# Optimization experiments

Hardware: AMD Instinct MI355X
Metric: run time of the kernel (lower is better)

## Reference

```python
import jax, jax.numpy as jnp
import numpy as np

B, N, C = 32, 262144, 5
ALPHA = 50.0
EPS_LS = 0.2
BASE_W = [0.8, 2.0, 1.5, 1.5, 3.5]
# (cid, ref, sign): height_diff = sign*(pr_z[cid] - gt_z[ref]); violation = sigmoid(-10*diff)
# Enumerates all z_above / z_below pairs in the hierarchy dict.
PAIRS = [(1, 2, -1.0), (1, 3, -1.0), (1, 4, -1.0),
         (2, 1, 1.0), (2, 3, -1.0), (2, 4, -1.0),
         (3, 1, 1.0), (3, 2, 1.0), (3, 4, -1.0),
         (4, 1, 1.0), (4, 2, 1.0), (4, 3, 1.0)]


def setup_inputs() -> dict:
    key = jax.random.key(0)
    k1, k2, k3 = jax.random.split(key, 3)
    outputs = jax.random.normal(k1, (B, C, N), dtype=jnp.float32)
    labels = jax.random.randint(k2, (B, N), 0, C, dtype=jnp.int32)
    points = jax.random.normal(k3, (B, N, 3), dtype=jnp.float32)
    return {"outputs": outputs, "labels": labels, "points": points}


def _centroid(points, mask):
    # points: [B,N,3], mask: [B,N] bool -> ([B,3], [B] valid)
    valid = mask.any(axis=1)
    m = mask.astype(points.dtype)
    s = jnp.einsum('bn,bnd->bd', m, points)
    cnt = jnp.clip(m.sum(axis=1), 1.0)
    return s / cnt[:, None], valid


def _forward(outputs, points, labels):
    logits = jnp.transpose(outputs, (0, 2, 1))  # [B,N,C]
    b = labels.shape[0]
    preds = jnp.argmax(logits, axis=-1)  # [B,N]
    base = jnp.asarray(BASE_W, dtype=logits.dtype)
    weights = jnp.broadcast_to(base, (b, C))
    gt_c = {cid: _centroid(points, labels == cid) for cid in (1, 2, 3, 4)}
    pr_c = {cid: _centroid(points, preds == cid) for cid in (1, 2, 3, 4)}
    # hierarchy violation scatter into per-batch class weights
    for cid, ref, sign in PAIRS:
        pr_pos, pos_valid = pr_c[cid]
        gt_ref, ref_valid = gt_c[ref]
        valid = ref_valid & pos_valid
        diff = sign * (pr_pos[:, 2] - gt_ref[:, 2])
        add = jnp.where(valid, ALPHA * jax.nn.sigmoid(-diff * 10.0), 0.0)
        weights = weights.at[:, cid].add(add).at[:, ref].add(0.3 * add)
    # predicted bounding boxes of masked points (zeros included, as in torch)
    bounds = {}
    for cid in (2, 3):
        mp = points * (preds == cid)[:, :, None].astype(points.dtype)
        bounds[cid] = jnp.stack([mp.min(axis=1), mp.max(axis=1)], axis=1)  # [B,2,3]
    for cid in (2, 3):
        rb = bounds[3 if cid == 2 else 2]
        xc = (bounds[cid][:, :, 0] - rb[:, 0:1, 0]) / (rb[:, 1:2, 0] - rb[:, 0:1, 0] + 1e-7)
        yc = (bounds[cid][:, :, 1] - rb[:, 0:1, 1]) / (rb[:, 1:2, 1] - rb[:, 0:1, 1] + 1e-7)
        viol = ((xc < 0.1) | (xc > 0.9)) | ((yc < 0.1) | (yc > 0.9))
        weights = weights.at[:, cid].add(ALPHA * viol.astype(weights.dtype).mean(axis=1))
    weights = jnp.clip(weights, 0.1, 10.0)
    # inverse-sqrt class frequency weights
    dist = jnp.bincount(labels.reshape(-1), length=C).astype(logits.dtype)
    cw = 1.0 / (jnp.sqrt(dist) + 1e-7)
    cw = cw / cw.sum() * C
    w = weights.mean(axis=0) * cw  # [C]
    # weighted cross entropy with label_smoothing=0.2 (PyTorch semantics)
    logp = jax.nn.log_softmax(logits.reshape(-1, C), axis=-1)
    y = labels.reshape(-1)
    wt = w[y]
    wsum = wt.sum()
    nll = (wt * -jnp.take_along_axis(logp, y[:, None], axis=1)[:, 0]).sum() / wsum
    smooth = (-(logp * w[None, :]).sum(axis=-1)).sum() / wsum
    return (1.0 - EPS_LS) * nll + (EPS_LS / C) * smooth


def reference(outputs, labels, points):
    return _forward(outputs, points, labels)
```

## Files before the change

### kernel.cpp

```cpp
#include <hip/hip_runtime.h>
#include <math.h>

#define NPTS 262144
#define BATCH 32
#define BPB 64
#define NBLK (BATCH * BPB)
#define NREP 8


__device__ __forceinline__ float wred_sum(float v) {
#pragma unroll
    for (int o = 32; o; o >>= 1) v += __shfl_down(v, o);
    return v;
}
__device__ __forceinline__ unsigned wred_usum(unsigned v) {
#pragma unroll
    for (int o = 32; o; o >>= 1) v += __shfl_down(v, o);
    return v;
}

__device__ __forceinline__ unsigned mapf(float f) {
    unsigned u = __float_as_uint(f);
    return (u & 0x80000000u) ? ~u : (u | 0x80000000u);
}
__device__ __forceinline__ float unmapf(unsigned m) {
    return (m & 0x80000000u) ? __uint_as_float(m ^ 0x80000000u)
                             : __uint_as_float(~m);
}

__global__ __launch_bounds__(256) void bsl_main(
    const float* __restrict__ outputs, const int* __restrict__ labels,
    const float* __restrict__ points,
    float* gsum, unsigned* gcnt, float* bsum, unsigned* bcnt,
    unsigned* bmn, unsigned* bmx, int iters)
{
    const int blk = blockIdx.x;
    const int b = blk / BPB;
    const int seg = blk % BPB;
    const int seg_start = seg * (iters * 1024);
    const int tid = threadIdx.x;

    float S[5] = {0, 0, 0, 0, 0};
    float T[5] = {0, 0, 0, 0, 0};
    float lseacc = 0.f;
    float gtz[4] = {0, 0, 0, 0};
    float prz[4] = {0, 0, 0, 0};
    const float INF = __int_as_float(0x7f800000);
    float mn2x = INF, mx2x = -INF, mn2y = INF, mx2y = -INF;
    float mn3x = INF, mx3x = -INF, mn3y = INF, mx3y = -INF;
    unsigned bc[5] = {0, 0, 0, 0, 0}, prc[4] = {0, 0, 0, 0};

    const float* obase = outputs + (size_t)b * 5 * NPTS;
    const int*   lbase = labels + (size_t)b * NPTS;
    const float* pbase = points + (size_t)b * NPTS * 3;

    for (int it = 0; it < iters; ++it) {
        const int n = seg_start + it * 1024 + tid * 4;
        float4 L[5];
#pragma unroll
        for (int c = 0; c < 5; ++c)
            L[c] = *(const float4*)(obase + (size_t)c * NPTS + n);
        const int4 lab = *(const int4*)(lbase + n);
        const float4* pp = (const float4*)(pbase + (size_t)n * 3);
        const float4 p0 = pp[0], p1 = pp[1], p2 = pp[2];
        const float xs[4] = {p0.x, p0.w, p1.z, p2.y};
        const float ys[4] = {p0.y, p1.x, p1.w, p2.z};
        const float zs[4] = {p0.z, p1.y, p2.x, p2.w};
        const int   lb[4] = {lab.x, lab.y, lab.z, lab.w};
#pragma unroll
        for (int j = 0; j < 4; ++j) {
            float v[5];
#pragma unroll
            for (int c = 0; c < 5; ++c) v[c] = ((const float*)&L[c])[j];
            float best = v[0]; int pred = 0;
#pragma unroll
            for (int c = 1; c < 5; ++c)
                if (v[c] > best) { best = v[c]; pred = c; }
            float e = 0.f;
#pragma unroll
            for (int c = 0; c < 5; ++c) e += __expf(v[c] - best);
            const float lse = best + __logf(e);
            lseacc += lse;
            const int y = lb[j];
#pragma unroll
            for (int c = 0; c < 5; ++c) {
                S[c] += v[c];
                const bool is = (y == c);
                T[c] += is ? (lse - v[c]) : 0.f;
                bc[c] += is ? 1u : 0u;
            }
            const float z = zs[j];
#pragma unroll
            for (int k = 0; k < 4; ++k) {
                const bool gy = (y == k + 1), py = (pred == k + 1);
                gtz[k] += gy ? z : 0.f;
                prz[k] += py ? z : 0.f;
                prc[k] += py ? 1u : 0u;
            }
            const float x = xs[j], yv = ys[j];
            const float a2x = (pred == 2) ? x : 0.f;
            const float a2y = (pred == 2) ? yv : 0.f;
            const float a3x = (pred == 3) ? x : 0.f;
            const float a3y = (pred == 3) ? yv : 0.f;
            mn2x = fminf(mn2x, a2x); mx2x = fmaxf(mx2x, a2x);
            mn2y = fminf(mn2y, a2y); mx2y = fmaxf(mx2y, a2y);
            mn3x = fminf(mn3x, a3x); mx3x = fmaxf(mx3x, a3x);
            mn3y = fminf(mn3y, a3y); mx3y = fmaxf(mx3y, a3y);
        }
    }

    float fv[27] = {S[0], S[1], S[2], S[3], S[4],
                    T[0], T[1], T[2], T[3], T[4],
                    lseacc,
                    gtz[0], gtz[1], gtz[2], gtz[3],
                    prz[0], prz[1], prz[2], prz[3],
                    mn2x, mx2x, mn2y, mx2y, mn3x, mx3x, mn3y, mx3y};
    unsigned iv[9] = {bc[0], bc[1], bc[2], bc[3], bc[4],
                      prc[0], prc[1], prc[2], prc[3]};

    __shared__ float sf[4][27];
    __shared__ unsigned si[4][9];
    const int wid = tid >> 6, lane = tid & 63;
#pragma unroll
    for (int vdx = 0; vdx < 27; ++vdx) {
        float r;
        if (vdx < 19) r = wred_sum(fv[vdx]);
        else if (((vdx - 19) & 1) == 0) {
#pragma unroll
            for (int o = 32; o; o >>= 1) fv[vdx] = fminf(fv[vdx], __shfl_down(fv[vdx], o));
            r = fv[vdx];
        } else {
#pragma unroll
            for (int o = 32; o; o >>= 1) fv[vdx] = fmaxf(fv[vdx], __shfl_down(fv[vdx], o));
            r = fv[vdx];
        }
        if (lane == 0) sf[wid][vdx] = r;
    }
#pragma unroll
    for (int vdx = 0; vdx < 9; ++vdx) {
        unsigned r = wred_usum(iv[vdx]);
        if (lane == 0) si[wid][vdx] = r;
    }
    __syncthreads();

    const int rep = blk & (NREP - 1);
    if (tid < 27) {
        float r = sf[0][tid];
        if (tid < 19) {
            r += sf[1][tid] + sf[2][tid] + sf[3][tid];
        } else if (((tid - 19) & 1) == 0) {
            r = fminf(fminf(r, sf[1][tid]), fminf(sf[2][tid], sf[3][tid]));
        } else {
            r = fmaxf(fmaxf(r, sf[1][tid]), fmaxf(sf[2][tid], sf[3][tid]));
        }
        if (tid < 11) {
            atomicAdd(&gsum[rep * 11 + tid], r);
        } else if (tid < 19) {
            atomicAdd(&bsum[b * 8 + (tid - 11)], r);
        } else {
            const int g = tid - 19;
            const unsigned m = mapf(r);
            if ((g & 1) == 0) atomicMin(&bmn[b * 4 + (g >> 1)], m);
            else              atomicMax(&bmx[b * 4 + (g >> 1)], m);
        }
    } else if (tid >= 32 && tid < 41) {
        const int v = tid - 32;
        const unsigned r = si[0][v] + si[1][v] + si[2][v] + si[3][v];
        if (v < 5) {
            atomicAdd(&gcnt[rep * 5 + v], r);
            if (v >= 1) atomicAdd(&bcnt[b * 8 + (v - 1)], r);
        } else {
            atomicAdd(&bcnt[b * 8 + 4 + (v - 5)], r);
        }
    }
}

__global__ __launch_bounds__(64) void bsl_final(
    const float* __restrict__ gsum, const unsigned* __restrict__ gcnt,
    const float* __restrict__ bsum, const unsigned* __restrict__ bcnt,
    const unsigned* __restrict__ bmn, const unsigned* __restrict__ bmx,
    float* __restrict__ out)
{
    const int lane = threadIdx.x;
    __shared__ float smg[16];

    if (lane < 16) {
        float s = 0.f;
        if (lane < 11) {
#pragma unroll
            for (int r = 0; r < NREP; ++r) s += gsum[r * 11 + lane];
        } else {
            unsigned u = 0;
#pragma unroll
            for (int r = 0; r < NREP; ++r) u += gcnt[r * 5 + (lane - 11)];
            s = (float)u;
        }
        smg[lane] = s;
    }

    const float BASE_W[5] = {0.8f, 2.0f, 1.5f, 1.5f, 3.5f};
    const int pc[12]  = {1, 1, 1, 2, 2, 2, 3, 3, 3, 4, 4, 4};
    const int prf[12] = {2, 3, 4, 1, 3, 4, 1, 2, 4, 1, 2, 3};
    const float ps[12] = {-1.f, -1.f, -1.f, 1.f, -1.f, -1.f, 1.f, 1.f, -1.f, 1.f, 1.f, 1.f};

    float w[5] = {0, 0, 0, 0, 0};
    if (lane < BATCH) {
        for (int c = 0; c < 5; ++c) w[c] = BASE_W[c];
        float gtm[4], prm[4];
        bool gv[4], pv[4];
#pragma unroll
        for (int k = 0; k < 4; ++k) {
            const unsigned c1 = bcnt[lane * 8 + k];
            gv[k] = (c1 > 0u);
            gtm[k] = bsum[lane * 8 + k] / fmaxf((float)c1, 1.f);
            const unsigned c2 = bcnt[lane * 8 + 4 + k];
            pv[k] = (c2 > 0u);
            prm[k] = bsum[lane * 8 + 4 + k] / fmaxf((float)c2, 1.f);
        }
#pragma unroll
        for (int p = 0; p < 12; ++p) {
            const int cid = pc[p], ref = prf[p];
            float add = 0.f;
            if (pv[cid - 1] && gv[ref - 1]) {
                const float diff = ps[p] * (prm[cid - 1] - gtm[ref - 1]);
                add = 50.f / (1.f + expf(10.f * diff));
            }
            w[cid] += add;
            w[ref] += 0.3f * add;
        }
        const float mn2x = unmapf(bmn[lane * 4 + 0]), mx2x = unmapf(bmx[lane * 4 + 0]);
        const float mn2y = unmapf(bmn[lane * 4 + 1]), mx2y = unmapf(bmx[lane * 4 + 1]);
        const float mn3x = unmapf(bmn[lane * 4 + 2]), mx3x = unmapf(bmx[lane * 4 + 2]);
        const float mn3y = unmapf(bmn[lane * 4 + 3]), mx3y = unmapf(bmx[lane * 4 + 3]);
        {
            const float dx = mx3x - mn3x + 1e-7f, dy = mx3y - mn3y + 1e-7f;
            const float xc0 = (mn2x - mn3x) / dx, xc1 = (mx2x - mn3x) / dx;
            const float yc0 = (mn2y - mn3y) / dy, yc1 = (mx2y - mn3y) / dy;
            const float v0 = (xc0 < 0.1f || xc0 > 0.9f || yc0 < 0.1f || yc0 > 0.9f) ? 1.f : 0.f;
            const float v1 = (xc1 < 0.1f || xc1 > 0.9f || yc1 < 0.1f || yc1 > 0.9f) ? 1.f : 0.f;
            w[2] += 50.f * 0.5f * (v0 + v1);
        }
        {
            const float dx = mx2x - mn2x + 1e-7f, dy = mx2y - mn2y + 1e-7f;
            const float xc0 = (mn3x - mn2x) / dx, xc1 = (mx3x - mn2x) / dx;
            const float yc0 = (mn3y - mn2y) / dy, yc1 = (mx3y - mn2y) / dy;
            const float v0 = (xc0 < 0.1f || xc0 > 0.9f || yc0 < 0.1f || yc0 > 0.9f) ? 1.f : 0.f;
            const float v1 = (xc1 < 0.1f || xc1 > 0.9f || yc1 < 0.1f || yc1 > 0.9f) ? 1.f : 0.f;
            w[3] += 50.f * 0.5f * (v0 + v1);
        }
#pragma unroll
        for (int c = 0; c < 5; ++c)
            w[c] = fminf(fmaxf(w[c], 0.1f), 10.f);
    }
    float wsumc[5];
#pragma unroll
    for (int c = 0; c < 5; ++c) wsumc[c] = wred_sum(w[c]);

    __syncthreads();
    if (lane == 0) {
        float dist[5], cw[5], s = 0.f;
#pragma unroll
        for (int c = 0; c < 5; ++c) {
            dist[c] = smg[11 + c];
            cw[c] = 1.f / (sqrtf(dist[c]) + 1e-7f);
            s += cw[c];
        }
        float wf[5], wsum = 0.f, W = 0.f, nllnum = 0.f, Ssum = 0.f;
#pragma unroll
        for (int c = 0; c < 5; ++c) {
            cw[c] = cw[c] / s * 5.f;
            wf[c] = (wsumc[c] / 32.f) * cw[c];
            wsum += wf[c] * dist[c];
            W += wf[c];
            nllnum += wf[c] * smg[5 + c];
            Ssum += wf[c] * smg[c];
        }
        const float nll = nllnum / wsum;
        const float smooth = (W * smg[10] - Ssum) / wsum;
        out[0] = 0.8f * nll + 0.04f * smooth;
    }
}

extern "C" void kernel_launch(void* const* d_in, const int* in_sizes, int n_in,
                              void* d_out, int out_size, void* d_ws, size_t ws_size,
                              hipStream_t stream) {
    const float* outputs = (const float*)d_in[0];
    const int*   labels  = (const int*)d_in[1];
    const float* points  = (const float*)d_in[2];
    float* out = (float*)d_out;

    char* base = (char*)d_ws;
    float*    gsum = (float*)(base + 0);
    unsigned* gcnt = (unsigned*)(base + 352);
    float*    bsum = (float*)(base + 512);
    unsigned* bcnt = (unsigned*)(base + 1536);
    unsigned* bmx  = (unsigned*)(base + 2560);
    unsigned* bmn  = (unsigned*)(base + 3072);

    const int iters = NPTS / (BPB * 1024);

    hipMemsetAsync(base, 0, 3072, stream);
    hipMemsetAsync(base + 3072, 0xFF, 512, stream);
    bsl_main<<<NBLK, 256, 0, stream>>>(outputs, labels, points,
                                       gsum, gcnt, bsum, bcnt, bmn, bmx, iters);
    bsl_final<<<1, 64, 0, stream>>>(gsum, gcnt, bsum, bcnt, bmn, bmx, out);
}
```

Baseline: 71.89 us.

## Software-pipeline loads with double buffering, fewer blocks, single memset via negated max

Reduces blocks per batch from 64 to 16 so each block does 16 fixed iterations. Loads are double-buffered: the next group is prefetched while the current one is processed, with the loop fully unrolled. Min reductions become atomicMax on the mapped negated value, which allows one zeroing memset instead of two. The aim is to hide memory latency and cut launch and atomic overhead, at the cost of higher register pressure and fewer waves to hide latency.

After: 192.3 us. 167% more time.

```diff
diff --git a/kernel.cpp b/kernel.cpp
--- a/kernel.cpp
+++ b/kernel.cpp
@@ -3,8 +3,9 @@
 
 #define NPTS 262144
 #define BATCH 32
-#define BPB 64
+#define BPB 16
 #define NBLK (BATCH * BPB)
+#define ITERS 16
 #define NREP 8
 
 
@@ -26,97 +27,130 @@
 __device__ __forceinline__ float unmapf(unsigned m) {
     return (m & 0x80000000u) ? __uint_as_float(m ^ 0x80000000u)
                              : __uint_as_float(~m);
+}
+
+struct Grp {
+    float4 L0, L1, L2, L3, L4;
+    int4   lab;
+    float4 p0, p1, p2;
+};
+
+__device__ __forceinline__ Grp ldgrp(const float* __restrict__ obase,
+                                     const int* __restrict__ lbase,
+                                     const float* __restrict__ pbase, int n) {
+    Grp g;
+    g.L0 = *(const float4*)(obase + (size_t)0 * NPTS + n);
+    g.L1 = *(const float4*)(obase + (size_t)1 * NPTS + n);
+    g.L2 = *(const float4*)(obase + (size_t)2 * NPTS + n);
+    g.L3 = *(const float4*)(obase + (size_t)3 * NPTS + n);
+    g.L4 = *(const float4*)(obase + (size_t)4 * NPTS + n);
+    g.lab = *(const int4*)(lbase + n);
+    const float4* pp = (const float4*)(pbase + (size_t)n * 3);
+    g.p0 = pp[0]; g.p1 = pp[1]; g.p2 = pp[2];
+    return g;
+}
+
+struct Acc {
+    float S[5], T[5], lse;
+    float gtz[4], prz[4];
+    float mn2x, mx2x, mn2y, mx2y, mn3x, mx3x, mn3y, mx3y;
+    unsigned bc[5], prc[4];
+};
+
+__device__ __forceinline__ void process(const Grp& g, Acc& a) {
+    const float xs[4] = {g.p0.x, g.p0.w, g.p1.z, g.p2.y};
+    const float ys[4] = {g.p0.y, g.p1.x, g.p1.w, g.p2.z};
+    const float zs[4] = {g.p0.z, g.p1.y, g.p2.x, g.p2.w};
+    const int   lb[4] = {g.lab.x, g.lab.y, g.lab.z, g.lab.w};
+#pragma unroll
+    for (int j = 0; j < 4; ++j) {
+        float v[5];
+        v[0] = ((const float*)&g.L0)[j];
+        v[1] = ((const float*)&g.L1)[j];
+        v[2] = ((const float*)&g.L2)[j];
+        v[3] = ((const float*)&g.L3)[j];
+        v[4] = ((const float*)&g.L4)[j];
+        float best = v[0]; int pred = 0;
+#pragma unroll
+        for (int c = 1; c < 5; ++c)
+            if (v[c] > best) { best = v[c]; pred = c; }
+        float e = 0.f;
+#pragma unroll
+        for (int c = 0; c < 5; ++c) e += __expf(v[c] - best);
+        const float lse = best + __logf(e);
+        a.lse += lse;
+        const int y = lb[j];
+#pragma unroll
+        for (int c = 0; c < 5; ++c) {
+            a.S[c] += v[c];
+            const bool is = (y == c);
+            a.T[c] += is ? (lse - v[c]) : 0.f;
+            a.bc[c] += is ? 1u : 0u;
+        }
+        const float z = zs[j];
+#pragma unroll
+        for (int k = 0; k < 4; ++k) {
+            const bool gy = (y == k + 1), py = (pred == k + 1);
+            a.gtz[k] += gy ? z : 0.f;
+            a.prz[k] += py ? z : 0.f;
+            a.prc[k] += py ? 1u : 0u;
+        }
+        const float x = xs[j], yv = ys[j];
+        const float a2x = (pred == 2) ? x : 0.f;
+        const float a2y = (pred == 2) ? yv : 0.f;
+        const float a3x = (pred == 3) ? x : 0.f;
+        const float a3y = (pred == 3) ? yv : 0.f;
+        a.mn2x = fminf(a.mn2x, a2x); a.mx2x = fmaxf(a.mx2x, a2x);
+        a.mn2y = fminf(a.mn2y, a2y); a.mx2y = fmaxf(a.mx2y, a2y);
+        a.mn3x = fminf(a.mn3x, a3x); a.mx3x = fmaxf(a.mx3x, a3x);
+        a.mn3y = fminf(a.mn3y, a3y); a.mx3y = fmaxf(a.mx3y, a3y);
+    }
 }
 
 __global__ __launch_bounds__(256) void bsl_main(
     const float* __restrict__ outputs, const int* __restrict__ labels,
     const float* __restrict__ points,
     float* gsum, unsigned* gcnt, float* bsum, unsigned* bcnt,
-    unsigned* bmn, unsigned* bmx, int iters)
+    unsigned* bmn, unsigned* bmx)
 {
     const int blk = blockIdx.x;
     const int b = blk / BPB;
     const int seg = blk % BPB;
-    const int seg_start = seg * (iters * 1024);
     const int tid = threadIdx.x;
-
-    float S[5] = {0, 0, 0, 0, 0};
-    float T[5] = {0, 0, 0, 0, 0};
-    float lseacc = 0.f;
-    float gtz[4] = {0, 0, 0, 0};
-    float prz[4] = {0, 0, 0, 0};
+    const int base_n = seg * (ITERS * 1024) + tid * 4;
+
+    Acc a;
+#pragma unroll
+    for (int c = 0; c < 5; ++c) { a.S[c] = 0.f; a.T[c] = 0.f; a.bc[c] = 0u; }
+    a.lse = 0.f;
+#pragma unroll
+    for (int k = 0; k < 4; ++k) { a.gtz[k] = 0.f; a.prz[k] = 0.f; a.prc[k] = 0u; }
     const float INF = __int_as_float(0x7f800000);
-    float mn2x = INF, mx2x = -INF, mn2y = INF, mx2y = -INF;
-    float mn3x = INF, mx3x = -INF, mn3y = INF, mx3y = -INF;
-    unsigned bc[5] = {0, 0, 0, 0, 0}, prc[4] = {0, 0, 0, 0};
+    a.mn2x = INF; a.mx2x = -INF; a.mn2y = INF; a.mx2y = -INF;
+    a.mn3x = INF; a.mx3x = -INF; a.mn3y = INF; a.mx3y = -INF;
 
     const float* obase = outputs + (size_t)b * 5 * NPTS;
     const int*   lbase = labels + (size_t)b * NPTS;
     const float* pbase = points + (size_t)b * NPTS * 3;
 
-    for (int it = 0; it < iters; ++it) {
-        const int n = seg_start + it * 1024 + tid * 4;
-        float4 L[5];
-#pragma unroll
-        for (int c = 0; c < 5; ++c)
-            L[c] = *(const float4*)(obase + (size_t)c * NPTS + n);
-        const int4 lab = *(const int4*)(lbase + n);
-        const float4* pp = (const float4*)(pbase + (size_t)n * 3);
-        const float4 p0 = pp[0], p1 = pp[1], p2 = pp[2];
-        const float xs[4] = {p0.x, p0.w, p1.z, p2.y};
-        const float ys[4] = {p0.y, p1.x, p1.w, p2.z};
-        const float zs[4] = {p0.z, p1.y, p2.x, p2.w};
-        const int   lb[4] = {lab.x, lab.y, lab.z, lab.w};
-#pragma unroll
-        for (int j = 0; j < 4; ++j) {
-            float v[5];
-#pragma unroll
-            for (int c = 0; c < 5; ++c) v[c] = ((const float*)&L[c])[j];
-            float best = v[0]; int pred = 0;
-#pragma unroll
-            for (int c = 1; c < 5; ++c)
-                if (v[c] > best) { best = v[c]; pred = c; }
-            float e = 0.f;
-#pragma unroll
-            for (int c = 0; c < 5; ++c) e += __expf(v[c] - best);
-            const float lse = best + __logf(e);
-            lseacc += lse;
-            const int y = lb[j];
-#pragma unroll
-            for (int c = 0; c < 5; ++c) {
-                S[c] += v[c];
-                const bool is = (y == c);
-                T[c] += is ? (lse - v[c]) : 0.f;
-                bc[c] += is ? 1u : 0u;
-            }
-            const float z = zs[j];
-#pragma unroll
-            for (int k = 0; k < 4; ++k) {
-                const bool gy = (y == k + 1), py = (pred == k + 1);
-                gtz[k] += gy ? z : 0.f;
-                prz[k] += py ? z : 0.f;
-                prc[k] += py ? 1u : 0u;
-            }
-            const float x = xs[j], yv = ys[j];
-            const float a2x = (pred == 2) ? x : 0.f;
-            const float a2y = (pred == 2) ? yv : 0.f;
-            const float a3x = (pred == 3) ? x : 0.f;
-            const float a3y = (pred == 3) ? yv : 0.f;
-            mn2x = fminf(mn2x, a2x); mx2x = fmaxf(mx2x, a2x);
-            mn2y = fminf(mn2y, a2y); mx2y = fmaxf(mx2y, a2y);
-            mn3x = fminf(mn3x, a3x); mx3x = fmaxf(mx3x, a3x);
-            mn3y = fminf(mn3y, a3y); mx3y = fmaxf(mx3y, a3y);
-        }
-    }
-
-    float fv[27] = {S[0], S[1], S[2], S[3], S[4],
-                    T[0], T[1], T[2], T[3], T[4],
-                    lseacc,
-                    gtz[0], gtz[1], gtz[2], gtz[3],
-                    prz[0], prz[1], prz[2], prz[3],
-                    mn2x, mx2x, mn2y, mx2y, mn3x, mx3x, mn3y, mx3y};
-    unsigned iv[9] = {bc[0], bc[1], bc[2], bc[3], bc[4],
-                      prc[0], prc[1], prc[2], prc[3]};
+    Grp gA = ldgrp(obase, lbase, pbase, base_n);
+    Grp gB = ldgrp(obase, lbase, pbase, base_n + 1024);
+#pragma unroll
+    for (int it = 0; it < ITERS; it += 2) {
+        process(gA, a);
+        if (it + 2 < ITERS) gA = ldgrp(obase, lbase, pbase, base_n + (it + 2) * 1024);
+        process(gB, a);
+        if (it + 3 < ITERS) gB = ldgrp(obase, lbase, pbase, base_n + (it + 3) * 1024);
+    }
+
+    float fv[27] = {a.S[0], a.S[1], a.S[2], a.S[3], a.S[4],
+                    a.T[0], a.T[1], a.T[2], a.T[3], a.T[4],
+                    a.lse,
+                    a.gtz[0], a.gtz[1], a.gtz[2], a.gtz[3],
+                    a.prz[0], a.prz[1], a.prz[2], a.prz[3],
+                    a.mn2x, a.mx2x, a.mn2y, a.mx2y, a.mn3x, a.mx3x, a.mn3y, a.mx3y};
+    unsigned iv[9] = {a.bc[0], a.bc[1], a.bc[2], a.bc[3], a.bc[4],
+                      a.prc[0], a.prc[1], a.prc[2], a.prc[3]};
 
     __shared__ float sf[4][27];
     __shared__ unsigned si[4][9];
@@ -159,9 +193,8 @@
             atomicAdd(&bsum[b * 8 + (tid - 11)], r);
         } else {
             const int g = tid - 19;
-            const unsigned m = mapf(r);
-            if ((g & 1) == 0) atomicMin(&bmn[b * 4 + (g >> 1)], m);
-            else              atomicMax(&bmx[b * 4 + (g >> 1)], m);
+            if ((g & 1) == 0) atomicMax(&bmn[b * 4 + (g >> 1)], mapf(-r));
+            else              atomicMax(&bmx[b * 4 + (g >> 1)], mapf(r));
         }
     } else if (tid >= 32 && tid < 41) {
         const int v = tid - 32;
@@ -228,10 +261,10 @@
             w[cid] += add;
             w[ref] += 0.3f * add;
         }
-        const float mn2x = unmapf(bmn[lane * 4 + 0]), mx2x = unmapf(bmx[lane * 4 + 0]);
-        const float mn2y = unmapf(bmn[lane * 4 + 1]), mx2y = unmapf(bmx[lane * 4 + 1]);
-        const float mn3x = unmapf(bmn[lane * 4 + 2]), mx3x = unmapf(bmx[lane * 4 + 2]);
-        const float mn3y = unmapf(bmn[lane * 4 + 3]), mx3y = unmapf(bmx[lane * 4 + 3]);
+        const float mn2x = -unmapf(bmn[lane * 4 + 0]), mx2x = unmapf(bmx[lane * 4 + 0]);
+        const float mn2y = -unmapf(bmn[lane * 4 + 1]), mx2y = unmapf(bmx[lane * 4 + 1]);
+        const float mn3x = -unmapf(bmn[lane * 4 + 2]), mx3x = unmapf(bmx[lane * 4 + 2]);
+        const float mn3y = -unmapf(bmn[lane * 4 + 3]), mx3y = unmapf(bmx[lane * 4 + 3]);
         {
             const float dx = mx3x - mn3x + 1e-7f, dy = mx3y - mn3y + 1e-7f;
             const float xc0 = (mn2x - mn3x) / dx, xc1 = (mx2x - mn3x) / dx;
@@ -297,11 +330,8 @@
     unsigned* bmx  = (unsigned*)(base + 2560);
     unsigned* bmn  = (unsigned*)(base + 3072);
 
-    const int iters = NPTS / (BPB * 1024);
-
-    hipMemsetAsync(base, 0, 3072, stream);
-    hipMemsetAsync(base + 3072, 0xFF, 512, stream);
+    hipMemsetAsync(base, 0, 3584, stream);
     bsl_main<<<NBLK, 256, 0, stream>>>(outputs, labels, points,
-                                       gsum, gcnt, bsum, bcnt, bmn, bmx, iters);
+                                       gsum, gcnt, bsum, bcnt, bmn, bmx);
     bsl_final<<<1, 64, 0, stream>>>(gsum, gcnt, bsum, bcnt, bmn, bmx, out);
 }
```
